# Kernel optimization log

Measured on AMD Instinct MI355X. Metric: run time of the kernel, lower is better.

The kernel has to match this reference:

```python
import jax, jax.numpy as jnp
import numpy as np

B, N, D, E = 4, 16384, 128, 1048576  # batch, nodes/graph, hidden, total edges


def setup_inputs() -> dict:
    key = jax.random.key(0)
    k0, k1, k2, k3, k4, k5, k6 = jax.random.split(key, 7)
    x = jax.random.normal(k0, (B, N, D), dtype=jnp.float32)
    W = jax.random.normal(k1, (D, D), dtype=jnp.float32) * 0.05  # 'random_normal' init
    b = jax.random.normal(k2, (D,), dtype=jnp.float32) * 0.05
    edge_b = jax.random.randint(k3, (E,), 0, B, dtype=jnp.int32)
    edge_row = jax.random.randint(k4, (E,), 0, N, dtype=jnp.int32)
    edge_col = jax.random.randint(k5, (E,), 0, N, dtype=jnp.int32)
    edge_vals = jax.random.uniform(k6, (E,), dtype=jnp.float32)
    return {"x": x, "W": W, "b": b, "edge_b": edge_b, "edge_row": edge_row,
            "edge_col": edge_col, "edge_vals": edge_vals, "k": 2}


def reference(x, W, b, edge_b, edge_row, edge_col, edge_vals, k):
    # adj is a batched sparse [B, N, N]; edges stored as (batch, row, col, val) COO.
    seg_row = edge_b * N + edge_row  # flattened destination id in [0, B*N)
    # in_degrees = sum_j |adj[b, i, j]|
    deg = jax.ops.segment_sum(jnp.abs(edge_vals), seg_row, num_segments=B * N)
    deg = deg.reshape(B, N)
    norm = jnp.power(deg + 1e-6, -0.5)[..., None]          # [B, N, 1]
    norm_k = jnp.power(norm, k)                             # computed but unused (faithful to source)
    support = jnp.einsum('bnd,de->bne', x, W)               # x @ W
    y = (support * norm).reshape(B * N, D)                  # pre-normalized features
    # SpMM: out[b, i] = sum_{(b,i,j)} adj_val * y[b, j]
    msgs = y[edge_b * N + edge_col] * edge_vals[:, None]    # [E, D] gather + scale
    agg = jax.ops.segment_sum(msgs, seg_row, num_segments=B * N).reshape(B, N, D)
    return jax.nn.relu(agg * norm + b)
```

## Files before the change

kernel.cpp:

```cpp
#include <hip/hip_runtime.h>
#include <stdint.h>

#define B_ 4
#define N_ 16384
#define D_ 128
#define E_ 1048576
#define BN_ 65536
#define NBKT 256
#define NBLK 256
#define CAP  6144
#define CAPQ 1536

typedef __attribute__((ext_vector_type(8))) short short8;
typedef __attribute__((ext_vector_type(4))) float floatx4;

static constexpr size_t OFF_Y      = 0;
static constexpr size_t OFF_PACK1  = 16777216;
static constexpr size_t OFF_GBKT   = OFF_PACK1 + 12582912;
static constexpr size_t OFF_NORM   = OFF_GBKT + 1024;
static constexpr size_t OFF_ROWST  = OFF_NORM + 262144;
static constexpr size_t OFF_WH     = OFF_ROWST + 262144;
static constexpr size_t OFF_WL     = OFF_WH + 32768;

__device__ __forceinline__ uint32_t rne16(uint32_t u) {
    return (u + 0x7FFFu + ((u >> 16) & 1u)) >> 16;
}
__device__ __forceinline__ void bf16split(float f, uint16_t& h, uint16_t& l) {
    uint32_t hb = rne16(__float_as_uint(f));
    h = (uint16_t)hb;
    float r = f - __uint_as_float(hb << 16);
    l = (uint16_t)rne16(__float_as_uint(r));
}

__global__ __launch_bounds__(1024, 2) void k_scatter(const int* __restrict__ eb,
                                                     const int* __restrict__ er,
                                                     const int* __restrict__ ec,
                                                     const float* __restrict__ ev,
                                                     const float* __restrict__ Wg,
                                                     uint32_t* __restrict__ gbkt,
                                                     uint2* __restrict__ pack1,
                                                     uint16_t* __restrict__ WhG,
                                                     uint16_t* __restrict__ WlG) {
    __shared__ uint32_t h[NBKT];
    int t = threadIdx.x;
    if (t < NBKT) h[t] = 0;
    if (blockIdx.x < 16) {
        int g = blockIdx.x * 1024 + t;
        float w = Wg[g];
        uint16_t hh, ll;
        bf16split(w, hh, ll);
        int k = g >> 7, n = g & 127;
        int o = ((k >> 3) * 128 + n) * 8 + (k & 7);
        WhG[o] = hh;
        WlG[o] = ll;
    }
    __syncthreads();
    int vbase = blockIdx.x * 1024 + t;
    int4   b4 = ((const int4*)eb)[vbase];
    int4   r4 = ((const int4*)er)[vbase];
    int4   c4 = ((const int4*)ec)[vbase];
    float4 v4 = ((const float4*)ev)[vbase];
    uint32_t k0 = (uint32_t)(b4.x * N_ + r4.x);
    uint32_t k1 = (uint32_t)(b4.y * N_ + r4.y);
    uint32_t k2 = (uint32_t)(b4.z * N_ + r4.z);
    uint32_t k3 = (uint32_t)(b4.w * N_ + r4.w);
    atomicAdd(&h[k0 >> 8], 1u);
    atomicAdd(&h[k1 >> 8], 1u);
    atomicAdd(&h[k2 >> 8], 1u);
    atomicAdd(&h[k3 >> 8], 1u);
    __syncthreads();
    if (t < NBKT) {
        uint32_t c = h[t];
        uint32_t base = c ? atomicAdd(&gbkt[t], c) : 0u;
        h[t] = base;
    }
    __syncthreads();
    {
        uint32_t off = atomicAdd(&h[k0 >> 8], 1u);
        pack1[(size_t)(k0 >> 8) * CAP + off] =
            make_uint2(((k0 & 255u) << 14) | (uint32_t)c4.x, __float_as_uint(v4.x));
    }
    {
        uint32_t off = atomicAdd(&h[k1 >> 8], 1u);
        pack1[(size_t)(k1 >> 8) * CAP + off] =
            make_uint2(((k1 & 255u) << 14) | (uint32_t)c4.y, __float_as_uint(v4.y));
    }
    {
        uint32_t off = atomicAdd(&h[k2 >> 8], 1u);
        pack1[(size_t)(k2 >> 8) * CAP + off] =
            make_uint2(((k2 & 255u) << 14) | (uint32_t)c4.z, __float_as_uint(v4.z));
    }
    {
        uint32_t off = atomicAdd(&h[k3 >> 8], 1u);
        pack1[(size_t)(k3 >> 8) * CAP + off] =
            make_uint2(((k3 & 255u) << 14) | (uint32_t)c4.w, __float_as_uint(v4.w));
    }
}

__global__ __launch_bounds__(1024) void k_degsort(const uint32_t* __restrict__ gbkt,
                                                  const uint2* __restrict__ pack1,
                                                  float* __restrict__ norm,
                                                  uint32_t* __restrict__ rowst) {
    __shared__ float    dsum[NBKT];
    __shared__ uint32_t cnt[NBKT];
    __shared__ uint32_t scn[NBKT];
    int t = threadIdx.x;
    int bkt = blockIdx.x;
    if (t < NBKT) { dsum[t] = 0.f; cnt[t] = 0; }
    __syncthreads();
    uint32_t n = gbkt[bkt];
    size_t bstart = (size_t)bkt * CAP;
    for (uint32_t i = t; i < n; i += 1024) {
        uint2 p = pack1[bstart + i];
        uint32_t nl = p.x >> 14;
        atomicAdd(&cnt[nl], 1u);
        atomicAdd(&dsum[nl], fabsf(__uint_as_float(p.y)));
    }
    __syncthreads();
    if (t < NBKT) scn[t] = cnt[t];
    __syncthreads();
    for (int off = 1; off < NBKT; off <<= 1) {
        uint32_t a = 0;
        if (t < NBKT && t >= off) a = scn[t - off];
        __syncthreads();
        if (t < NBKT) scn[t] += a;
        __syncthreads();
    }
    if (t < NBKT) {
        norm[bkt * NBKT + t] = rsqrtf(dsum[t] + 1e-6f);
        rowst[bkt * NBKT + t] = scn[t] - cnt[t];
    }
}

__global__ __launch_bounds__(256) void k_matmul_mfma(const float* __restrict__ x,
                                                     const uint16_t* __restrict__ WhG,
                                                     const uint16_t* __restrict__ WlG,
                                                     const float* __restrict__ norm,
                                                     uint32_t* __restrict__ ybf) {
    __shared__ short WhS[16384];
    __shared__ short WlS[16384];
    __shared__ short XhS[4096];
    __shared__ short XlS[4096];
    __shared__ float normS[32];
    int tid = threadIdx.x;
    int row0 = blockIdx.x * 32;

    {
        const uint4* whg = (const uint4*)WhG;
        const uint4* wlg = (const uint4*)WlG;
        uint4* whs = (uint4*)WhS;
        uint4* wls = (uint4*)WlS;
#pragma unroll
        for (int i = 0; i < 8; ++i) {
            whs[i * 256 + tid] = whg[i * 256 + tid];
            wls[i * 256 + tid] = wlg[i * 256 + tid];
        }
    }
#pragma unroll
    for (int cc = 0; cc < 2; ++cc) {
        int c = cc * 256 + tid;
        int m = c & 31, kk = c >> 5;
        const float4* xp = (const float4*)(x + (size_t)(row0 + m) * D_ + kk * 8);
        float4 f0 = xp[0], f1 = xp[1];
        union { short8 v; uint16_t s[8]; } uh, ul;
        bf16split(f0.x, uh.s[0], ul.s[0]); bf16split(f0.y, uh.s[1], ul.s[1]);
        bf16split(f0.z, uh.s[2], ul.s[2]); bf16split(f0.w, uh.s[3], ul.s[3]);
        bf16split(f1.x, uh.s[4], ul.s[4]); bf16split(f1.y, uh.s[5], ul.s[5]);
        bf16split(f1.z, uh.s[6], ul.s[6]); bf16split(f1.w, uh.s[7], ul.s[7]);
        ((short8*)XhS)[c] = uh.v;
        ((short8*)XlS)[c] = ul.v;
    }
    if (tid < 32) normS[tid] = norm[row0 + tid];
    __syncthreads();

    int lane = tid & 63;
    int wv = tid >> 6;
    int quad = lane >> 4;
    int l15 = lane & 15;
    int wcol0 = wv * 32;
    floatx4 acc[2][2] = {};
    const short8* Xh8 = (const short8*)XhS;
    const short8* Xl8 = (const short8*)XlS;
    const short8* Wh8 = (const short8*)WhS;
    const short8* Wl8 = (const short8*)WlS;
#pragma unroll
    for (int ks = 0; ks < 4; ++ks) {
        int kkq = ks * 4 + quad;
        short8 ah0 = Xh8[kkq * 32 + l15];
        short8 ah1 = Xh8[kkq * 32 + 16 + l15];
        short8 al0 = Xl8[kkq * 32 + l15];
        short8 al1 = Xl8[kkq * 32 + 16 + l15];
        short8 bh0 = Wh8[kkq * 128 + wcol0 + l15];
        short8 bh1 = Wh8[kkq * 128 + wcol0 + 16 + l15];
        short8 bl0 = Wl8[kkq * 128 + wcol0 + l15];
        short8 bl1 = Wl8[kkq * 128 + wcol0 + 16 + l15];
        acc[0][0] = __builtin_amdgcn_mfma_f32_16x16x32_bf16(ah0, bh0, acc[0][0], 0, 0, 0);
        acc[0][1] = __builtin_amdgcn_mfma_f32_16x16x32_bf16(ah0, bh1, acc[0][1], 0, 0, 0);
        acc[1][0] = __builtin_amdgcn_mfma_f32_16x16x32_bf16(ah1, bh0, acc[1][0], 0, 0, 0);
        acc[1][1] = __builtin_amdgcn_mfma_f32_16x16x32_bf16(ah1, bh1, acc[1][1], 0, 0, 0);
        acc[0][0] = __builtin_amdgcn_mfma_f32_16x16x32_bf16(ah0, bl0, acc[0][0], 0, 0, 0);
        acc[0][1] = __builtin_amdgcn_mfma_f32_16x16x32_bf16(ah0, bl1, acc[0][1], 0, 0, 0);
        acc[1][0] = __builtin_amdgcn_mfma_f32_16x16x32_bf16(ah1, bl0, acc[1][0], 0, 0, 0);
        acc[1][1] = __builtin_amdgcn_mfma_f32_16x16x32_bf16(ah1, bl1, acc[1][1], 0, 0, 0);
        acc[0][0] = __builtin_amdgcn_mfma_f32_16x16x32_bf16(al0, bh0, acc[0][0], 0, 0, 0);
        acc[0][1] = __builtin_amdgcn_mfma_f32_16x16x32_bf16(al0, bh1, acc[0][1], 0, 0, 0);
        acc[1][0] = __builtin_amdgcn_mfma_f32_16x16x32_bf16(al1, bh0, acc[1][0], 0, 0, 0);
        acc[1][1] = __builtin_amdgcn_mfma_f32_16x16x32_bf16(al1, bh1, acc[1][1], 0, 0, 0);
    }

#pragma unroll
    for (int rt = 0; rt < 2; ++rt) {
#pragma unroll
        for (int ct = 0; ct < 2; ++ct) {
            floatx4 v = acc[rt][ct];
            int rbase = rt * 16 + quad * 4;
            int cp = (wcol0 + ct * 16) / 2 + (l15 >> 1);
#pragma unroll
            for (int r = 0; r < 4; ++r) {
                float mine = v[r] * normS[rbase + r];
                float oth = __shfl_xor(mine, 1, 64);
                uint32_t a = __float_as_uint((lane & 1) ? oth : mine);
                uint32_t b = __float_as_uint((lane & 1) ? mine : oth);
                uint32_t packed = rne16(a) | (rne16(b) << 16);
                bool doit = ((lane & 1) == 0) ? (r < 2) : (r >= 2);
                if (doit)
                    ybf[(size_t)(row0 + rbase + r) * 64 + cp] = packed;
            }
        }
    }
}

__device__ __forceinline__ void fma8(float* acc, float v, uint4 u) {
    acc[0] = fmaf(v, __uint_as_float(u.x << 16), acc[0]);
    acc[1] = fmaf(v, __uint_as_float(u.x & 0xFFFF0000u), acc[1]);
    acc[2] = fmaf(v, __uint_as_float(u.y << 16), acc[2]);
    acc[3] = fmaf(v, __uint_as_float(u.y & 0xFFFF0000u), acc[3]);
    acc[4] = fmaf(v, __uint_as_float(u.z << 16), acc[4]);
    acc[5] = fmaf(v, __uint_as_float(u.z & 0xFFFF0000u), acc[5]);
    acc[6] = fmaf(v, __uint_as_float(u.w << 16), acc[6]);
    acc[7] = fmaf(v, __uint_as_float(u.w & 0xFFFF0000u), acc[7]);
}

__global__ __launch_bounds__(512, 8) void k_spmm(const uint32_t* __restrict__ gbkt,
                                                 const uint2* __restrict__ pack1,
                                                 const uint32_t* __restrict__ rowst,
                                                 const uint4* __restrict__ y4,
                                                 const float* __restrict__ norm,
                                                 const float* __restrict__ bias,
                                                 float* __restrict__ out) {
    __shared__ uint2    srt[CAPQ];
    __shared__ uint32_t rs[65];
    __shared__ uint32_t rcur[64];
    int t = threadIdx.x;
    int blk = blockIdx.x;
    int xcd = blk & 7;
    int batch = xcd & 3;
    int qhi = xcd >> 2;
    int j = blk >> 3;
    int quarter = qhi * 2 + (j & 1);
    int bkt = batch * 64 + (j >> 1);
    int nbase = quarter * 64;
    uint32_t n = gbkt[bkt];
    if (t < 64) { rs[t] = rowst[bkt * NBKT + nbase + t]; rcur[t] = 0; }
    if (t == 64) rs[64] = (quarter == 3) ? n : rowst[bkt * NBKT + nbase + 64];
    __syncthreads();
    uint32_t qbase = rs[0];
    size_t base = (size_t)bkt * CAP;
    for (uint32_t i = t; i < n; i += 512) {
        uint2 p = pack1[base + i];
        uint32_t nl = p.x >> 14;
        if ((int)(nl >> 6) == quarter) {
            uint32_t loc = nl & 63;
            uint32_t pos = rs[loc] - qbase + atomicAdd(&rcur[loc], 1u);
            srt[pos] = p;
        }
    }
    __syncthreads();

    int wv = t >> 6;
    int lane = t & 63;
    int esub = lane >> 4;
    int chunk = lane & 15;
    uint32_t colbase = (uint32_t)batch << 14;
#pragma unroll 1
    for (int i = 0; i < 8; ++i) {
        int nl = wv * 8 + i;
        uint32_t e = rs[nl] - qbase;
        uint32_t end = rs[nl + 1] - qbase;
        float acc[8] = {0.f,0.f,0.f,0.f,0.f,0.f,0.f,0.f};
        for (; e + 16 <= end; e += 16) {
            uint2 pa = srt[e + esub];
            uint2 pb = srt[e + 4 + esub];
            uint2 pc = srt[e + 8 + esub];
            uint2 pd = srt[e + 12 + esub];
            uint4 ua = y4[(size_t)(colbase | (pa.x & 0x3FFFu)) * 16 + chunk];
            uint4 ub = y4[(size_t)(colbase | (pb.x & 0x3FFFu)) * 16 + chunk];
            uint4 uc = y4[(size_t)(colbase | (pc.x & 0x3FFFu)) * 16 + chunk];
            uint4 ud = y4[(size_t)(colbase | (pd.x & 0x3FFFu)) * 16 + chunk];
            fma8(acc, __uint_as_float(pa.y), ua);
            fma8(acc, __uint_as_float(pb.y), ub);
            fma8(acc, __uint_as_float(pc.y), uc);
            fma8(acc, __uint_as_float(pd.y), ud);
        }
        for (; e + 4 <= end; e += 4) {
            uint2 p = srt[e + esub];
            uint4 u = y4[(size_t)(colbase | (p.x & 0x3FFFu)) * 16 + chunk];
            fma8(acc, __uint_as_float(p.y), u);
        }
        if (e < end) {
            uint32_t idx = e + esub;
            bool act = idx < end;
            uint2 p = srt[act ? idx : (end - 1)];
            uint4 u = y4[(size_t)(colbase | (p.x & 0x3FFFu)) * 16 + chunk];
            float v = act ? __uint_as_float(p.y) : 0.f;
            fma8(acc, v, u);
        }
#pragma unroll
        for (int jj = 0; jj < 8; ++jj) {
            acc[jj] += __shfl_xor(acc[jj], 16, 64);
            acc[jj] += __shfl_xor(acc[jj], 32, 64);
        }
        if (esub < 2) {
            int node = bkt * NBKT + nbase + nl;
            float nm = norm[node];
            float4 bb = ((const float4*)bias)[chunk * 2 + esub];
            float4 o;
            o.x = fmaxf(fmaf(acc[esub * 4 + 0], nm, bb.x), 0.f);
            o.y = fmaxf(fmaf(acc[esub * 4 + 1], nm, bb.y), 0.f);
            o.z = fmaxf(fmaf(acc[esub * 4 + 2], nm, bb.z), 0.f);
            o.w = fmaxf(fmaf(acc[esub * 4 + 3], nm, bb.w), 0.f);
            ((float4*)out)[(size_t)node * 32 + chunk * 2 + esub] = o;
        }
    }
}

extern "C" void kernel_launch(void* const* d_in, const int* in_sizes, int n_in,
                              void* d_out, int out_size, void* d_ws, size_t ws_size,
                              hipStream_t stream) {
    const float* x  = (const float*)d_in[0];
    const float* W  = (const float*)d_in[1];
    const float* bi = (const float*)d_in[2];
    const int* eb   = (const int*)d_in[3];
    const int* er   = (const int*)d_in[4];
    const int* ec   = (const int*)d_in[5];
    const float* ev = (const float*)d_in[6];
    float* out = (float*)d_out;

    char* ws = (char*)d_ws;
    uint32_t* ybf    = (uint32_t*)(ws + OFF_Y);
    uint2*    pack1  = (uint2*)(ws + OFF_PACK1);
    uint32_t* gbkt   = (uint32_t*)(ws + OFF_GBKT);
    float*    norm   = (float*)(ws + OFF_NORM);
    uint32_t* rowst  = (uint32_t*)(ws + OFF_ROWST);
    uint16_t* WhG    = (uint16_t*)(ws + OFF_WH);
    uint16_t* WlG    = (uint16_t*)(ws + OFF_WL);

    hipMemsetAsync(gbkt, 0, NBKT * sizeof(uint32_t), stream);
    k_scatter<<<NBLK, 1024, 0, stream>>>(eb, er, ec, ev, W, gbkt, pack1, WhG, WlG);
    k_degsort<<<NBKT, 1024, 0, stream>>>(gbkt, pack1, norm, rowst);
    k_matmul_mfma<<<BN_ / 32, 256, 0, stream>>>(x, WhG, WlG, norm, ybf);
    k_spmm   <<<1024, 512, 0, stream>>>(gbkt, pack1, rowst, (const uint4*)ybf, norm, bi, out);
}
```

Measured before the change: 179.6 us.

## Bucket edges into 64-row buckets and drop memset via self-resetting counters

Edges are now scattered into 1024 buckets of 64 rows instead of 256 buckets of 256 rows, with capacity CAPQ per bucket. Each SpMM block therefore reads only its own bucket rather than scanning a 256-row bucket and filtering a quarter of it, which removes about three quarters of the redundant pack1 reads. Degree sorting runs on 1024 smaller blocks. The bucket counters move to a device global that SpMM resets at the end, which removes the memset launch. The cost is that correctness now depends on every bucket fitting in CAPQ (1536) and on the counters being zero before the first call.

```diff
diff --git a/kernel.cpp b/kernel.cpp
--- a/kernel.cpp
+++ b/kernel.cpp
@@ -6,9 +6,8 @@
 #define D_ 128
 #define E_ 1048576
 #define BN_ 65536
-#define NBKT 256
+#define NQB 1024
 #define NBLK 256
-#define CAP  6144
 #define CAPQ 1536
 
 typedef __attribute__((ext_vector_type(8))) short short8;
@@ -16,11 +15,12 @@
 
 static constexpr size_t OFF_Y      = 0;
 static constexpr size_t OFF_PACK1  = 16777216;
-static constexpr size_t OFF_GBKT   = OFF_PACK1 + 12582912;
-static constexpr size_t OFF_NORM   = OFF_GBKT + 1024;
+static constexpr size_t OFF_NORM   = OFF_PACK1 + 12582912;
 static constexpr size_t OFF_ROWST  = OFF_NORM + 262144;
 static constexpr size_t OFF_WH     = OFF_ROWST + 262144;
 static constexpr size_t OFF_WL     = OFF_WH + 32768;
+
+__device__ uint32_t gbkt_dev[NQB];
 
 __device__ __forceinline__ uint32_t rne16(uint32_t u) {
     return (u + 0x7FFFu + ((u >> 16) & 1u)) >> 16;
@@ -37,13 +37,12 @@
                                                      const int* __restrict__ ec,
                                                      const float* __restrict__ ev,
                                                      const float* __restrict__ Wg,
-                                                     uint32_t* __restrict__ gbkt,
                                                      uint2* __restrict__ pack1,
                                                      uint16_t* __restrict__ WhG,
                                                      uint16_t* __restrict__ WlG) {
-    __shared__ uint32_t h[NBKT];
+    __shared__ uint32_t h[NQB];
     int t = threadIdx.x;
-    if (t < NBKT) h[t] = 0;
+    h[t] = 0;
     if (blockIdx.x < 16) {
         int g = blockIdx.x * 1024 + t;
         float w = Wg[g];
@@ -64,71 +63,70 @@
     uint32_t k1 = (uint32_t)(b4.y * N_ + r4.y);
     uint32_t k2 = (uint32_t)(b4.z * N_ + r4.z);
     uint32_t k3 = (uint32_t)(b4.w * N_ + r4.w);
-    atomicAdd(&h[k0 >> 8], 1u);
-    atomicAdd(&h[k1 >> 8], 1u);
-    atomicAdd(&h[k2 >> 8], 1u);
-    atomicAdd(&h[k3 >> 8], 1u);
-    __syncthreads();
-    if (t < NBKT) {
+    atomicAdd(&h[k0 >> 6], 1u);
+    atomicAdd(&h[k1 >> 6], 1u);
+    atomicAdd(&h[k2 >> 6], 1u);
+    atomicAdd(&h[k3 >> 6], 1u);
+    __syncthreads();
+    {
         uint32_t c = h[t];
-        uint32_t base = c ? atomicAdd(&gbkt[t], c) : 0u;
+        uint32_t base = c ? atomicAdd(&gbkt_dev[t], c) : 0u;
         h[t] = base;
     }
     __syncthreads();
     {
-        uint32_t off = atomicAdd(&h[k0 >> 8], 1u);
-        pack1[(size_t)(k0 >> 8) * CAP + off] =
-            make_uint2(((k0 & 255u) << 14) | (uint32_t)c4.x, __float_as_uint(v4.x));
-    }
-    {
-        uint32_t off = atomicAdd(&h[k1 >> 8], 1u);
-        pack1[(size_t)(k1 >> 8) * CAP + off] =
-            make_uint2(((k1 & 255u) << 14) | (uint32_t)c4.y, __float_as_uint(v4.y));
-    }
-    {
-        uint32_t off = atomicAdd(&h[k2 >> 8], 1u);
-        pack1[(size_t)(k2 >> 8) * CAP + off] =
-            make_uint2(((k2 & 255u) << 14) | (uint32_t)c4.z, __float_as_uint(v4.z));
-    }
-    {
-        uint32_t off = atomicAdd(&h[k3 >> 8], 1u);
-        pack1[(size_t)(k3 >> 8) * CAP + off] =
-            make_uint2(((k3 & 255u) << 14) | (uint32_t)c4.w, __float_as_uint(v4.w));
-    }
-}
-
-__global__ __launch_bounds__(1024) void k_degsort(const uint32_t* __restrict__ gbkt,
-                                                  const uint2* __restrict__ pack1,
-                                                  float* __restrict__ norm,
-                                                  uint32_t* __restrict__ rowst) {
-    __shared__ float    dsum[NBKT];
-    __shared__ uint32_t cnt[NBKT];
-    __shared__ uint32_t scn[NBKT];
+        uint32_t off = atomicAdd(&h[k0 >> 6], 1u);
+        pack1[(size_t)(k0 >> 6) * CAPQ + off] =
+            make_uint2(((k0 & 63u) << 14) | (uint32_t)c4.x, __float_as_uint(v4.x));
+    }
+    {
+        uint32_t off = atomicAdd(&h[k1 >> 6], 1u);
+        pack1[(size_t)(k1 >> 6) * CAPQ + off] =
+            make_uint2(((k1 & 63u) << 14) | (uint32_t)c4.y, __float_as_uint(v4.y));
+    }
+    {
+        uint32_t off = atomicAdd(&h[k2 >> 6], 1u);
+        pack1[(size_t)(k2 >> 6) * CAPQ + off] =
+            make_uint2(((k2 & 63u) << 14) | (uint32_t)c4.z, __float_as_uint(v4.z));
+    }
+    {
+        uint32_t off = atomicAdd(&h[k3 >> 6], 1u);
+        pack1[(size_t)(k3 >> 6) * CAPQ + off] =
+            make_uint2(((k3 & 63u) << 14) | (uint32_t)c4.w, __float_as_uint(v4.w));
+    }
+}
+
+__global__ __launch_bounds__(256, 8) void k_degsort(const uint2* __restrict__ pack1,
+                                                    float* __restrict__ norm,
+                                                    uint32_t* __restrict__ rowst) {
+    __shared__ float    dsum[64];
+    __shared__ uint32_t cnt[64];
+    __shared__ uint32_t scn[64];
     int t = threadIdx.x;
-    int bkt = blockIdx.x;
-    if (t < NBKT) { dsum[t] = 0.f; cnt[t] = 0; }
-    __syncthreads();
-    uint32_t n = gbkt[bkt];
-    size_t bstart = (size_t)bkt * CAP;
-    for (uint32_t i = t; i < n; i += 1024) {
-        uint2 p = pack1[bstart + i];
+    int qb = blockIdx.x;
+    if (t < 64) { dsum[t] = 0.f; cnt[t] = 0; }
+    __syncthreads();
+    uint32_t n = gbkt_dev[qb];
+    size_t base = (size_t)qb * CAPQ;
+    for (uint32_t i = t; i < n; i += 256) {
+        uint2 p = pack1[base + i];
         uint32_t nl = p.x >> 14;
         atomicAdd(&cnt[nl], 1u);
         atomicAdd(&dsum[nl], fabsf(__uint_as_float(p.y)));
     }
     __syncthreads();
-    if (t < NBKT) scn[t] = cnt[t];
-    __syncthreads();
-    for (int off = 1; off < NBKT; off <<= 1) {
+    if (t < 64) scn[t] = cnt[t];
+    __syncthreads();
+    for (int off = 1; off < 64; off <<= 1) {
         uint32_t a = 0;
-        if (t < NBKT && t >= off) a = scn[t - off];
+        if (t < 64 && t >= off) a = scn[t - off];
         __syncthreads();
-        if (t < NBKT) scn[t] += a;
+        if (t < 64) scn[t] += a;
         __syncthreads();
     }
-    if (t < NBKT) {
-        norm[bkt * NBKT + t] = rsqrtf(dsum[t] + 1e-6f);
-        rowst[bkt * NBKT + t] = scn[t] - cnt[t];
+    if (t < 64) {
+        norm[qb * 64 + t] = rsqrtf(dsum[t] + 1e-6f);
+        rowst[qb * 64 + t] = scn[t] - cnt[t];
     }
 }
 
@@ -241,8 +239,7 @@
     acc[7] = fmaf(v, __uint_as_float(u.w & 0xFFFF0000u), acc[7]);
 }
 
-__global__ __launch_bounds__(512, 8) void k_spmm(const uint32_t* __restrict__ gbkt,
-                                                 const uint2* __restrict__ pack1,
+__global__ __launch_bounds__(512, 8) void k_spmm(const uint2* __restrict__ pack1,
                                                  const uint32_t* __restrict__ rowst,
                                                  const uint4* __restrict__ y4,
                                                  const float* __restrict__ norm,
@@ -255,25 +252,18 @@
     int blk = blockIdx.x;
     int xcd = blk & 7;
     int batch = xcd & 3;
-    int qhi = xcd >> 2;
-    int j = blk >> 3;
-    int quarter = qhi * 2 + (j & 1);
-    int bkt = batch * 64 + (j >> 1);
-    int nbase = quarter * 64;
-    uint32_t n = gbkt[bkt];
-    if (t < 64) { rs[t] = rowst[bkt * NBKT + nbase + t]; rcur[t] = 0; }
-    if (t == 64) rs[64] = (quarter == 3) ? n : rowst[bkt * NBKT + nbase + 64];
-    __syncthreads();
-    uint32_t qbase = rs[0];
-    size_t base = (size_t)bkt * CAP;
+    int local = ((xcd >> 2) << 7) | (blk >> 3);
+    int qb = (batch << 8) | local;
+    uint32_t n = gbkt_dev[qb];
+    if (t < 64) { rs[t] = rowst[qb * 64 + t]; rcur[t] = 0; }
+    if (t == 64) rs[64] = n;
+    __syncthreads();
+    size_t base = (size_t)qb * CAPQ;
     for (uint32_t i = t; i < n; i += 512) {
         uint2 p = pack1[base + i];
         uint32_t nl = p.x >> 14;
-        if ((int)(nl >> 6) == quarter) {
-            uint32_t loc = nl & 63;
-            uint32_t pos = rs[loc] - qbase + atomicAdd(&rcur[loc], 1u);
-            srt[pos] = p;
-        }
+        uint32_t pos = rs[nl] + atomicAdd(&rcur[nl], 1u);
+        srt[pos] = p;
     }
     __syncthreads();
 
@@ -285,8 +275,8 @@
 #pragma unroll 1
     for (int i = 0; i < 8; ++i) {
         int nl = wv * 8 + i;
-        uint32_t e = rs[nl] - qbase;
-        uint32_t end = rs[nl + 1] - qbase;
+        uint32_t e = rs[nl];
+        uint32_t end = rs[nl + 1];
         float acc[8] = {0.f,0.f,0.f,0.f,0.f,0.f,0.f,0.f};
         for (; e + 16 <= end; e += 16) {
             uint2 pa = srt[e + esub];
@@ -321,7 +311,7 @@
             acc[jj] += __shfl_xor(acc[jj], 32, 64);
         }
         if (esub < 2) {
-            int node = bkt * NBKT + nbase + nl;
+            int node = qb * 64 + nl;
             float nm = norm[node];
             float4 bb = ((const float4*)bias)[chunk * 2 + esub];
             float4 o;
@@ -332,6 +322,7 @@
             ((float4*)out)[(size_t)node * 32 + chunk * 2 + esub] = o;
         }
     }
+    if (t == 0) gbkt_dev[qb] = 0;
 }
 
 extern "C" void kernel_launch(void* const* d_in, const int* in_sizes, int n_in,
@@ -349,15 +340,13 @@
     char* ws = (char*)d_ws;
     uint32_t* ybf    = (uint32_t*)(ws + OFF_Y);
     uint2*    pack1  = (uint2*)(ws + OFF_PACK1);
-    uint32_t* gbkt   = (uint32_t*)(ws + OFF_GBKT);
     float*    norm   = (float*)(ws + OFF_NORM);
     uint32_t* rowst  = (uint32_t*)(ws + OFF_ROWST);
     uint16_t* WhG    = (uint16_t*)(ws + OFF_WH);
     uint16_t* WlG    = (uint16_t*)(ws + OFF_WL);
 
-    hipMemsetAsync(gbkt, 0, NBKT * sizeof(uint32_t), stream);
-    k_scatter<<<NBLK, 1024, 0, stream>>>(eb, er, ec, ev, W, gbkt, pack1, WhG, WlG);
-    k_degsort<<<NBKT, 1024, 0, stream>>>(gbkt, pack1, norm, rowst);
+    k_scatter<<<NBLK, 1024, 0, stream>>>(eb, er, ec, ev, W, pack1, WhG, WlG);
+    k_degsort<<<NQB, 256, 0, stream>>>(pack1, norm, rowst);
     k_matmul_mfma<<<BN_ / 32, 256, 0, stream>>>(x, WhG, WlG, norm, ybf);
-    k_spmm   <<<1024, 512, 0, stream>>>(gbkt, pack1, rowst, (const uint4*)ybf, norm, bi, out);
-}
+    k_spmm   <<<NQB, 512, 0, stream>>>(pack1, rowst, (const uint4*)ybf, norm, bi, out);
+}
```

Result: no change. 179.9 us (+0.1%).
